# Performance work log

Hardware: AMD Instinct MI355X
Metric: run time of the kernel (lower is better)

## Reference

```python
import jax, jax.numpy as jnp
import numpy as np

B, NQ, NK = 16, 2048, 2048
KD, QD, KQ = 256, 256, 256
CLIP = 10.0


def setup_inputs() -> dict:
    key = jax.random.key(0)
    k1, k2, k3, k4, k5 = jax.random.split(key, 5)
    k_inputs = jax.random.normal(k1, (B, NK, KD), dtype=jnp.float32)
    q_inputs = jax.random.normal(k2, (B, NQ, QD), dtype=jnp.float32)
    adjancy = jax.random.randint(k3, (B, NQ, NK), 0, 2, dtype=jnp.int32)
    # Linear init in source: (rand - 0.5) * 0.05 -> uniform(-0.025, 0.025)
    Wk = jax.random.uniform(k4, (KD, KQ), dtype=jnp.float32, minval=-0.025, maxval=0.025)
    Wq = jax.random.uniform(k5, (QD, KQ), dtype=jnp.float32, minval=-0.025, maxval=0.025)
    return {"k_inputs": k_inputs, "q_inputs": q_inputs, "adjancy": adjancy, "Wk": Wk, "Wq": Wq}


def reference(k_inputs, q_inputs, adjancy, Wk, Wq):
    k = jnp.einsum("bnd,de->bne", k_inputs, Wk)          # [B, NK, KQ]
    q = jnp.einsum("bmd,de->bme", q_inputs, Wq)          # [B, NQ, KQ]
    scale = 1.0 / jnp.sqrt(jnp.asarray(KQ, dtype=q.dtype))
    scores = jnp.einsum("bme,bne->bmn", q, k) * scale     # [B, NQ, NK]
    scores = jnp.tanh(scores) * CLIP                      # clip is not None
    scores = jnp.where(adjancy.astype(bool), scores, -jnp.inf)
    return jax.nn.softmax(scores, axis=2)
```

## Files before the change

### kernel.cpp

```cpp
#include <hip/hip_runtime.h>

#define BATCH 16
#define NQ 2048
#define NK 2048
#define KD 256

typedef short s16x8 __attribute__((ext_vector_type(8)));
typedef __bf16 bf16x8 __attribute__((ext_vector_type(8)));
typedef float f32x16 __attribute__((ext_vector_type(16)));
typedef float f32x4 __attribute__((ext_vector_type(4)));

static __device__ __forceinline__ unsigned short f2bf(float f) {
  unsigned u = __builtin_bit_cast(unsigned, f);
  u += 0x7FFFu + ((u >> 16) & 1u);
  return (unsigned short)(u >> 16);
}

static __device__ __forceinline__ float bf2f(unsigned short h) {
  return __builtin_bit_cast(float, (unsigned)h << 16);
}

static __device__ __forceinline__ f32x16 mfma_bf16(s16x8 a, s16x8 b, f32x16 c) {
  return __builtin_amdgcn_mfma_f32_32x32x16_bf16(
      __builtin_bit_cast(bf16x8, a), __builtin_bit_cast(bf16x8, b), c, 0, 0, 0);
}

__global__ void prep_wt(const float* __restrict__ Wk, unsigned short* __restrict__ WkT,
                        const float* __restrict__ Wq, unsigned short* __restrict__ WqT) {
  const float* W = blockIdx.y ? Wq : Wk;
  unsigned short* WT = blockIdx.y ? WqT : WkT;
  float scale = blockIdx.y ? 0.0625f : 1.0f;
  int idx = blockIdx.x * 256 + threadIdx.x;
  int n = idx >> 8, k = idx & 255;
  WT[n * 256 + k] = f2bf(W[k * 256 + n] * scale);
}

__global__ __launch_bounds__(256, 2) void proj_kernel(
    const float* __restrict__ Xk, const unsigned short* __restrict__ WkT,
    unsigned short* __restrict__ Yk,
    const float* __restrict__ Xq, const unsigned short* __restrict__ WqT,
    unsigned short* __restrict__ Yq) {
  const float* X;
  const unsigned short* WT;
  unsigned short* Y;
  if (blockIdx.y == 0) { X = Xk; WT = WkT; Y = Yk; }
  else                 { X = Xq; WT = WqT; Y = Yq; }

  int tid = threadIdx.x;
  int wave = tid >> 6, lane = tid & 63;
  int l31 = lane & 31, kh = lane >> 5;
  int r0 = blockIdx.x * 128 + wave * 32;

  const float* xp = X + (size_t)(r0 + l31) * 256 + kh * 8;

  f32x16 acc[8];
#pragma unroll
  for (int ct = 0; ct < 8; ++ct)
#pragma unroll
    for (int i = 0; i < 16; ++i) acc[ct][i] = 0.0f;

#pragma unroll
  for (int kk = 0; kk < 16; ++kk) {
    f32x4 a0 = *(const f32x4*)(xp + kk * 16);
    f32x4 a1 = *(const f32x4*)(xp + kk * 16 + 4);
    s16x8 af;
#pragma unroll
    for (int j = 0; j < 4; ++j) {
      af[j]     = (short)f2bf(a0[j]);
      af[4 + j] = (short)f2bf(a1[j]);
    }
#pragma unroll
    for (int ct = 0; ct < 8; ++ct) {
      s16x8 bw = *(const s16x8*)(WT + (size_t)(ct * 32 + l31) * 256 + kk * 16 + kh * 8);
      acc[ct] = mfma_bf16(af, bw, acc[ct]);
    }
  }

  size_t gbase = (size_t)(r0 >> 5) * 16;
#pragma unroll
  for (int ct = 0; ct < 8; ++ct) {
    int ecol = ct * 32 + l31;
    size_t cbase = (gbase + (ecol >> 4)) * 64 * 8 + ((ecol >> 3) & 1) * 32 * 8 + (ecol & 7);
#pragma unroll
    for (int r = 0; r < 16; ++r) {
      int rrow = (r & 3) + 8 * (r >> 2) + 4 * kh;
      Y[cbase + rrow * 8] = f2bf(acc[ct][r]);
    }
  }
}

__global__ __launch_bounds__(512, 2) void attn_kernel(
    const unsigned short* __restrict__ Kf, const unsigned short* __restrict__ Qf,
    const int* __restrict__ adj, float* __restrict__ out) {
  int lin = blockIdx.y * 64 + blockIdx.x;
  int b  = (lin & 7) * 2 + ((lin >> 3) & 1);
  int qt = lin >> 4;
  int q0 = qt * 32;
  int tid = threadIdx.x;
  int wave = tid >> 6, lane = tid & 63;
  int l31 = lane & 31, kh = lane >> 5;
  int colbase = wave * 256;

  __shared__ unsigned lmask[8 * 256];
  __shared__ float wsum[8][32];
  __shared__ float rrecip[32];

  const unsigned short* qp = Qf + ((size_t)(b * 64 + qt) * 16) * 512;
  s16x8 aq[16];
#pragma unroll
  for (int kk = 0; kk < 16; ++kk)
    aq[kk] = *(const s16x8*)(qp + (kk * 64 + lane) * 8);

  const int* abase = adj + ((size_t)b * NQ + q0) * (size_t)NK + colbase + lane;
  unsigned* lm = lmask + wave * 256;
#pragma unroll
  for (int rg = 0; rg < 4; ++rg) {
    int av[8][4];
#pragma unroll
    for (int r8 = 0; r8 < 8; ++r8) {
      const int* ap = abase + (size_t)(rg * 8 + r8) * NK;
#pragma unroll
      for (int cc = 0; cc < 4; ++cc) av[r8][cc] = ap[cc * 64];
    }
#pragma unroll
    for (int r8 = 0; r8 < 8; ++r8) {
      unsigned long long b0 = __ballot(av[r8][0] != 0);
      unsigned long long b1 = __ballot(av[r8][1] != 0);
      unsigned long long b2 = __ballot(av[r8][2] != 0);
      unsigned long long b3 = __ballot(av[r8][3] != 0);
      if (lane < 8) {
        unsigned long long bb = (lane & 4) ? ((lane & 2) ? b3 : b2)
                                           : ((lane & 2) ? b1 : b0);
        unsigned word = (lane & 1) ? (unsigned)(bb >> 32) : (unsigned)bb;
        lm[(rg * 8 + r8) * 8 + lane] = word;
      }
    }
  }

  const unsigned short* kfb = Kf + ((size_t)b * 64 * 16) * 512;

  float rsum[16];
#pragma unroll
  for (int r = 0; r < 16; ++r) rsum[r] = 0.0f;

  s16x8 pst[8][2];
  unsigned bit = 1u << l31;

#pragma unroll
  for (int ct = 0; ct < 8; ++ct) {
    f32x16 acc;
#pragma unroll
    for (int i = 0; i < 16; ++i) acc[i] = 0.0f;

    const unsigned short* kpt = kfb + ((size_t)(wave * 8 + ct) * 16) * 512;
#pragma unroll
    for (int kk = 0; kk < 16; ++kk) {
      s16x8 bk = *(const s16x8*)(kpt + (kk * 64 + lane) * 8);
      acc = mfma_bf16(aq[kk], bk, acc);
    }

#pragma unroll
    for (int r = 0; r < 16; ++r) {
      int rrow = (r & 3) + 8 * (r >> 2) + 4 * kh;
      unsigned mw = lm[rrow * 8 + ct];
      float s = acc[r];
      float u  = __builtin_amdgcn_exp2f(s * 2.885390081777927f);
      float th = 1.0f - 2.0f * __builtin_amdgcn_rcpf(u + 1.0f);
      float e  = __builtin_amdgcn_exp2f((10.0f * th - 10.0f) * 1.44269504088896f);
      float p  = (mw & bit) ? e : 0.0f;
      rsum[r] += p;
      pst[ct][r >> 3][r & 7] = (short)f2bf(p);
    }
  }

#pragma unroll
  for (int r = 0; r < 16; ++r) {
    float v = rsum[r];
    v += __shfl_xor(v, 1);
    v += __shfl_xor(v, 2);
    v += __shfl_xor(v, 4);
    v += __shfl_xor(v, 8);
    v += __shfl_xor(v, 16);
    rsum[r] = v;
  }
  if (l31 == 0) {
#pragma unroll
    for (int r = 0; r < 16; ++r)
      wsum[wave][(r & 3) + 8 * (r >> 2) + 4 * kh] = rsum[r];
  }
  __syncthreads();
  if (tid < 32) {
    float s = 0.0f;
#pragma unroll
    for (int w = 0; w < 8; ++w) s += wsum[w][tid];
    rrecip[tid] = 1.0f / s;
  }
  __syncthreads();

  float rc[16];
#pragma unroll
  for (int r = 0; r < 16; ++r) rc[r] = rrecip[(r & 3) + 8 * (r >> 2) + 4 * kh];

  float* op = out + ((size_t)b * NQ + q0) * (size_t)NK + colbase + l31;
#pragma unroll
  for (int ct = 0; ct < 8; ++ct) {
#pragma unroll
    for (int r = 0; r < 16; ++r) {
      int rrow = (r & 3) + 8 * (r >> 2) + 4 * kh;
      float pf = bf2f((unsigned short)pst[ct][r >> 3][r & 7]);
      op[(size_t)rrow * NK + ct * 32] = pf * rc[r];
    }
  }
}

extern "C" void kernel_launch(void* const* d_in, const int* in_sizes, int n_in,
                              void* d_out, int out_size, void* d_ws, size_t ws_size,
                              hipStream_t stream) {
  const float* k_in = (const float*)d_in[0];
  const float* q_in = (const float*)d_in[1];
  const int* adj    = (const int*)d_in[2];
  const float* Wk   = (const float*)d_in[3];
  const float* Wq   = (const float*)d_in[4];
  float* out = (float*)d_out;

  char* ws = (char*)d_ws;
  unsigned short* WkT = (unsigned short*)(ws);
  unsigned short* WqT = (unsigned short*)(ws + (1u << 17));
  unsigned short* Kf  = (unsigned short*)(ws + (1u << 18));
  unsigned short* Qf  = (unsigned short*)(ws + (1u << 18) + (1u << 24));

  prep_wt<<<dim3(256, 2), 256, 0, stream>>>(Wk, WkT, Wq, WqT);

  proj_kernel<<<dim3(256, 2), 256, 0, stream>>>(k_in, WkT, Kf, q_in, WqT, Qf);

  attn_kernel<<<dim3(64, 16), 512, 0, stream>>>(Kf, Qf, adj, out);
}
```

Before: 260.5 us.

## Recompute attention scores in a second pass to cut registers and raise occupancy

The Q fragment moves from per-wave registers into shared memory, and the bf16 probability stash held between the row-sum pass and the output pass is dropped. The output pass now recomputes the QK^T MFMAs and the tanh/exp math instead of reading stored values. With far fewer live registers, launch bounds go from 2 to 4 blocks per CU to increase occupancy and hide memory latency. The cost is twice the MFMA and transcendental work plus repeated K loads from global memory and Q reads from LDS.

```diff
diff --git a/kernel.cpp b/kernel.cpp
--- a/kernel.cpp
+++ b/kernel.cpp
@@ -14,10 +14,6 @@
   unsigned u = __builtin_bit_cast(unsigned, f);
   u += 0x7FFFu + ((u >> 16) & 1u);
   return (unsigned short)(u >> 16);
-}
-
-static __device__ __forceinline__ float bf2f(unsigned short h) {
-  return __builtin_bit_cast(float, (unsigned)h << 16);
 }
 
 static __device__ __forceinline__ f32x16 mfma_bf16(s16x8 a, s16x8 b, f32x16 c) {
@@ -89,7 +85,7 @@
   }
 }
 
-__global__ __launch_bounds__(512, 2) void attn_kernel(
+__global__ __launch_bounds__(512, 4) void attn_kernel(
     const unsigned short* __restrict__ Kf, const unsigned short* __restrict__ Qf,
     const int* __restrict__ adj, float* __restrict__ out) {
   int lin = blockIdx.y * 64 + blockIdx.x;
@@ -101,15 +97,14 @@
   int l31 = lane & 31, kh = lane >> 5;
   int colbase = wave * 256;
 
+  __shared__ unsigned short qlds[16 * 512];
   __shared__ unsigned lmask[8 * 256];
   __shared__ float wsum[8][32];
   __shared__ float rrecip[32];
 
   const unsigned short* qp = Qf + ((size_t)(b * 64 + qt) * 16) * 512;
-  s16x8 aq[16];
-#pragma unroll
-  for (int kk = 0; kk < 16; ++kk)
-    aq[kk] = *(const s16x8*)(qp + (kk * 64 + lane) * 8);
+  ((s16x8*)qlds)[tid]       = ((const s16x8*)qp)[tid];
+  ((s16x8*)qlds)[tid + 512] = ((const s16x8*)qp)[tid + 512];
 
   const int* abase = adj + ((size_t)b * NQ + q0) * (size_t)NK + colbase + lane;
   unsigned* lm = lmask + wave * 256;
@@ -137,39 +132,36 @@
     }
   }
 
+  __syncthreads();
+
   const unsigned short* kfb = Kf + ((size_t)b * 64 * 16) * 512;
+  unsigned bit = 1u << l31;
 
   float rsum[16];
 #pragma unroll
   for (int r = 0; r < 16; ++r) rsum[r] = 0.0f;
-
-  s16x8 pst[8][2];
-  unsigned bit = 1u << l31;
 
 #pragma unroll
   for (int ct = 0; ct < 8; ++ct) {
     f32x16 acc;
 #pragma unroll
     for (int i = 0; i < 16; ++i) acc[i] = 0.0f;
-
     const unsigned short* kpt = kfb + ((size_t)(wave * 8 + ct) * 16) * 512;
 #pragma unroll
     for (int kk = 0; kk < 16; ++kk) {
+      s16x8 a  = *(const s16x8*)(qlds + (kk * 64 + lane) * 8);
       s16x8 bk = *(const s16x8*)(kpt + (kk * 64 + lane) * 8);
-      acc = mfma_bf16(aq[kk], bk, acc);
-    }
-
+      acc = mfma_bf16(a, bk, acc);
+    }
 #pragma unroll
     for (int r = 0; r < 16; ++r) {
       int rrow = (r & 3) + 8 * (r >> 2) + 4 * kh;
       unsigned mw = lm[rrow * 8 + ct];
-      float s = acc[r];
+      float s  = acc[r];
       float u  = __builtin_amdgcn_exp2f(s * 2.885390081777927f);
       float th = 1.0f - 2.0f * __builtin_amdgcn_rcpf(u + 1.0f);
       float e  = __builtin_amdgcn_exp2f((10.0f * th - 10.0f) * 1.44269504088896f);
-      float p  = (mw & bit) ? e : 0.0f;
-      rsum[r] += p;
-      pst[ct][r >> 3][r & 7] = (short)f2bf(p);
+      rsum[r] += (mw & bit) ? e : 0.0f;
     }
   }
 
@@ -204,11 +196,26 @@
   float* op = out + ((size_t)b * NQ + q0) * (size_t)NK + colbase + l31;
 #pragma unroll
   for (int ct = 0; ct < 8; ++ct) {
+    f32x16 acc;
+#pragma unroll
+    for (int i = 0; i < 16; ++i) acc[i] = 0.0f;
+    const unsigned short* kpt = kfb + ((size_t)(wave * 8 + ct) * 16) * 512;
+#pragma unroll
+    for (int kk = 0; kk < 16; ++kk) {
+      s16x8 a  = *(const s16x8*)(qlds + (kk * 64 + lane) * 8);
+      s16x8 bk = *(const s16x8*)(kpt + (kk * 64 + lane) * 8);
+      acc = mfma_bf16(a, bk, acc);
+    }
 #pragma unroll
     for (int r = 0; r < 16; ++r) {
       int rrow = (r & 3) + 8 * (r >> 2) + 4 * kh;
-      float pf = bf2f((unsigned short)pst[ct][r >> 3][r & 7]);
-      op[(size_t)rrow * NK + ct * 32] = pf * rc[r];
+      unsigned mw = lm[rrow * 8 + ct];
+      float s  = acc[r];
+      float u  = __builtin_amdgcn_exp2f(s * 2.885390081777927f);
+      float th = 1.0f - 2.0f * __builtin_amdgcn_rcpf(u + 1.0f);
+      float e  = __builtin_amdgcn_exp2f((10.0f * th - 10.0f) * 1.44269504088896f);
+      float p  = (mw & bit) ? e : 0.0f;
+      op[(size_t)rrow * NK + ct * 32] = p * rc[r];
     }
   }
 }
```

After: 905.9 us. 3.48x slower.

## Switch attention to 16x16 MFMA tiles with 16-row blocks and LDS-staged probabilities

Applied to the files above, without the earlier changes.

The attention kernel now handles 16 query rows per block instead of 32, using 16x16x32 bf16 MFMAs, and the launch grid doubles to match. The projection output layout is rearranged to fit the new fragment shape. Unnormalized probabilities are staged in LDS as packed bf16 instead of held in registers, and the tanh-plus-exp chain is folded into fewer operations. The aim is to cut register pressure and raise occupancy and parallelism, at the cost of re-reading each K tile twice as often overall and more LDS traffic.

```diff
diff --git a/kernel.cpp b/kernel.cpp
--- a/kernel.cpp
+++ b/kernel.cpp
@@ -3,12 +3,12 @@
 #define BATCH 16
 #define NQ 2048
 #define NK 2048
-#define KD 256
 
 typedef short s16x8 __attribute__((ext_vector_type(8)));
 typedef __bf16 bf16x8 __attribute__((ext_vector_type(8)));
 typedef float f32x16 __attribute__((ext_vector_type(16)));
 typedef float f32x4 __attribute__((ext_vector_type(4)));
+typedef unsigned u32x2 __attribute__((ext_vector_type(2)));
 
 static __device__ __forceinline__ unsigned short f2bf(float f) {
   unsigned u = __builtin_bit_cast(unsigned, f);
@@ -16,13 +16,19 @@
   return (unsigned short)(u >> 16);
 }
 
-static __device__ __forceinline__ float bf2f(unsigned short h) {
-  return __builtin_bit_cast(float, (unsigned)h << 16);
-}
-
-static __device__ __forceinline__ f32x16 mfma_bf16(s16x8 a, s16x8 b, f32x16 c) {
+static __device__ __forceinline__ f32x16 mfma32(s16x8 a, s16x8 b, f32x16 c) {
   return __builtin_amdgcn_mfma_f32_32x32x16_bf16(
       __builtin_bit_cast(bf16x8, a), __builtin_bit_cast(bf16x8, b), c, 0, 0, 0);
+}
+
+static __device__ __forceinline__ f32x4 mfma16(s16x8 a, s16x8 b, f32x4 c) {
+  return __builtin_amdgcn_mfma_f32_16x16x32_bf16(
+      __builtin_bit_cast(bf16x8, a), __builtin_bit_cast(bf16x8, b), c, 0, 0, 0);
+}
+
+static __device__ __forceinline__ float score_p(float s) {
+  float u = __builtin_amdgcn_exp2f(s * 2.885390081777927f);
+  return __builtin_amdgcn_exp2f(-28.853900817779268f * __builtin_amdgcn_rcpf(u + 1.0f));
 }
 
 __global__ void prep_wt(const float* __restrict__ Wk, unsigned short* __restrict__ WkT,
@@ -72,19 +78,19 @@
 #pragma unroll
     for (int ct = 0; ct < 8; ++ct) {
       s16x8 bw = *(const s16x8*)(WT + (size_t)(ct * 32 + l31) * 256 + kk * 16 + kh * 8);
-      acc[ct] = mfma_bf16(af, bw, acc[ct]);
-    }
-  }
-
-  size_t gbase = (size_t)(r0 >> 5) * 16;
+      acc[ct] = mfma32(af, bw, acc[ct]);
+    }
+  }
+
+  int kg2 = l31 >> 3, j = l31 & 7;
 #pragma unroll
   for (int ct = 0; ct < 8; ++ct) {
-    int ecol = ct * 32 + l31;
-    size_t cbase = (gbase + (ecol >> 4)) * 64 * 8 + ((ecol >> 3) & 1) * 32 * 8 + (ecol & 7);
 #pragma unroll
     for (int r = 0; r < 16; ++r) {
       int rrow = (r & 3) + 8 * (r >> 2) + 4 * kh;
-      Y[cbase + rrow * 8] = f2bf(acc[ct][r]);
+      int row = r0 + rrow;
+      Y[((size_t)((row >> 4) * 8 + ct) * 64 + kg2 * 16 + (row & 15)) * 8 + j] =
+          f2bf(acc[ct][r]);
     }
   }
 }
@@ -92,104 +98,88 @@
 __global__ __launch_bounds__(512, 2) void attn_kernel(
     const unsigned short* __restrict__ Kf, const unsigned short* __restrict__ Qf,
     const int* __restrict__ adj, float* __restrict__ out) {
-  int lin = blockIdx.y * 64 + blockIdx.x;
+  int lin = blockIdx.y * 128 + blockIdx.x;
   int b  = (lin & 7) * 2 + ((lin >> 3) & 1);
   int qt = lin >> 4;
-  int q0 = qt * 32;
+  int q0 = qt * 16;
   int tid = threadIdx.x;
   int wave = tid >> 6, lane = tid & 63;
-  int l31 = lane & 31, kh = lane >> 5;
+  int l15 = lane & 15, kg = lane >> 4;
   int colbase = wave * 256;
 
-  __shared__ unsigned lmask[8 * 256];
-  __shared__ float wsum[8][32];
-  __shared__ float rrecip[32];
-
-  const unsigned short* qp = Qf + ((size_t)(b * 64 + qt) * 16) * 512;
-  s16x8 aq[16];
-#pragma unroll
-  for (int kk = 0; kk < 16; ++kk)
-    aq[kk] = *(const s16x8*)(qp + (kk * 64 + lane) * 8);
+  __shared__ unsigned plds[8 * 16 * 64 * 2];
+  __shared__ unsigned lmask[8 * 144];
+  __shared__ float wsum[8][16];
+  __shared__ float rrecip[16];
+
+  const unsigned short* qp = Qf + (size_t)(b * 128 + qt) * 8 * 512;
+  s16x8 aq[8];
+#pragma unroll
+  for (int kk = 0; kk < 8; ++kk)
+    aq[kk] = *(const s16x8*)(qp + ((size_t)kk * 64 + lane) * 8);
 
   const int* abase = adj + ((size_t)b * NQ + q0) * (size_t)NK + colbase + lane;
-  unsigned* lm = lmask + wave * 256;
-#pragma unroll
-  for (int rg = 0; rg < 4; ++rg) {
-    int av[8][4];
-#pragma unroll
-    for (int r8 = 0; r8 < 8; ++r8) {
-      const int* ap = abase + (size_t)(rg * 8 + r8) * NK;
-#pragma unroll
-      for (int cc = 0; cc < 4; ++cc) av[r8][cc] = ap[cc * 64];
-    }
-#pragma unroll
-    for (int r8 = 0; r8 < 8; ++r8) {
-      unsigned long long b0 = __ballot(av[r8][0] != 0);
-      unsigned long long b1 = __ballot(av[r8][1] != 0);
-      unsigned long long b2 = __ballot(av[r8][2] != 0);
-      unsigned long long b3 = __ballot(av[r8][3] != 0);
-      if (lane < 8) {
-        unsigned long long bb = (lane & 4) ? ((lane & 2) ? b3 : b2)
-                                           : ((lane & 2) ? b1 : b0);
-        unsigned word = (lane & 1) ? (unsigned)(bb >> 32) : (unsigned)bb;
-        lm[(rg * 8 + r8) * 8 + lane] = word;
-      }
-    }
-  }
-
-  const unsigned short* kfb = Kf + ((size_t)b * 64 * 16) * 512;
-
-  float rsum[16];
-#pragma unroll
-  for (int r = 0; r < 16; ++r) rsum[r] = 0.0f;
-
-  s16x8 pst[8][2];
-  unsigned bit = 1u << l31;
-
-#pragma unroll
-  for (int ct = 0; ct < 8; ++ct) {
-    f32x16 acc;
-#pragma unroll
-    for (int i = 0; i < 16; ++i) acc[i] = 0.0f;
-
-    const unsigned short* kpt = kfb + ((size_t)(wave * 8 + ct) * 16) * 512;
-#pragma unroll
-    for (int kk = 0; kk < 16; ++kk) {
-      s16x8 bk = *(const s16x8*)(kpt + (kk * 64 + lane) * 8);
-      acc = mfma_bf16(aq[kk], bk, acc);
-    }
-
-#pragma unroll
-    for (int r = 0; r < 16; ++r) {
-      int rrow = (r & 3) + 8 * (r >> 2) + 4 * kh;
-      unsigned mw = lm[rrow * 8 + ct];
-      float s = acc[r];
-      float u  = __builtin_amdgcn_exp2f(s * 2.885390081777927f);
-      float th = 1.0f - 2.0f * __builtin_amdgcn_rcpf(u + 1.0f);
-      float e  = __builtin_amdgcn_exp2f((10.0f * th - 10.0f) * 1.44269504088896f);
-      float p  = (mw & bit) ? e : 0.0f;
-      rsum[r] += p;
-      pst[ct][r >> 3][r & 7] = (short)f2bf(p);
-    }
-  }
-
+  unsigned* lm = lmask + wave * 144;
 #pragma unroll
   for (int r = 0; r < 16; ++r) {
+    const int* ap = abase + (size_t)r * NK;
+    int a0 = ap[0], a1 = ap[64], a2 = ap[128], a3 = ap[192];
+    unsigned long long b0 = __ballot(a0 != 0);
+    unsigned long long b1 = __ballot(a1 != 0);
+    unsigned long long b2 = __ballot(a2 != 0);
+    unsigned long long b3 = __ballot(a3 != 0);
+    if (lane < 8) {
+      unsigned long long bb = (lane & 4) ? ((lane & 2) ? b3 : b2)
+                                         : ((lane & 2) ? b1 : b0);
+      unsigned word = (lane & 1) ? (unsigned)(bb >> 32) : (unsigned)bb;
+      lm[r * 9 + lane] = word;
+    }
+  }
+
+  const unsigned short* kfb = Kf + (size_t)b * 128 * 8 * 512;
+  unsigned* pl = plds + (wave * 16) * 128 + lane * 2;
+
+  float rsum[4] = {0.0f, 0.0f, 0.0f, 0.0f};
+
+#pragma unroll 2
+  for (int ct = 0; ct < 16; ++ct) {
+    f32x4 acc = {0.0f, 0.0f, 0.0f, 0.0f};
+    const unsigned short* kpt = kfb + (size_t)(wave * 16 + ct) * 8 * 512;
+#pragma unroll
+    for (int kk = 0; kk < 8; ++kk) {
+      s16x8 bk = *(const s16x8*)(kpt + ((size_t)kk * 64 + lane) * 8);
+      acc = mfma16(aq[kk], bk, acc);
+    }
+    unsigned shift = (unsigned)((ct & 1) * 16 + l15);
+    float p[4];
+#pragma unroll
+    for (int r = 0; r < 4; ++r) {
+      unsigned mw = lm[(kg * 4 + r) * 9 + (ct >> 1)];
+      float e = score_p(acc[r]);
+      p[r] = ((mw >> shift) & 1u) ? e : 0.0f;
+      rsum[r] += p[r];
+    }
+    unsigned lo = (unsigned)f2bf(p[0]) | ((unsigned)f2bf(p[1]) << 16);
+    unsigned hi = (unsigned)f2bf(p[2]) | ((unsigned)f2bf(p[3]) << 16);
+    u32x2 v; v[0] = lo; v[1] = hi;
+    *(u32x2*)(pl + ct * 128) = v;
+  }
+
+#pragma unroll
+  for (int r = 0; r < 4; ++r) {
     float v = rsum[r];
     v += __shfl_xor(v, 1);
     v += __shfl_xor(v, 2);
     v += __shfl_xor(v, 4);
     v += __shfl_xor(v, 8);
-    v += __shfl_xor(v, 16);
     rsum[r] = v;
   }
-  if (l31 == 0) {
-#pragma unroll
-    for (int r = 0; r < 16; ++r)
-      wsum[wave][(r & 3) + 8 * (r >> 2) + 4 * kh] = rsum[r];
+  if (l15 == 0) {
+#pragma unroll
+    for (int r = 0; r < 4; ++r) wsum[wave][kg * 4 + r] = rsum[r];
   }
   __syncthreads();
-  if (tid < 32) {
+  if (tid < 16) {
     float s = 0.0f;
 #pragma unroll
     for (int w = 0; w < 8; ++w) s += wsum[w][tid];
@@ -197,19 +187,22 @@
   }
   __syncthreads();
 
-  float rc[16];
-#pragma unroll
-  for (int r = 0; r < 16; ++r) rc[r] = rrecip[(r & 3) + 8 * (r >> 2) + 4 * kh];
-
-  float* op = out + ((size_t)b * NQ + q0) * (size_t)NK + colbase + l31;
-#pragma unroll
-  for (int ct = 0; ct < 8; ++ct) {
-#pragma unroll
-    for (int r = 0; r < 16; ++r) {
-      int rrow = (r & 3) + 8 * (r >> 2) + 4 * kh;
-      float pf = bf2f((unsigned short)pst[ct][r >> 3][r & 7]);
-      op[(size_t)rrow * NK + ct * 32] = pf * rc[r];
-    }
+  float rc[4];
+#pragma unroll
+  for (int r = 0; r < 4; ++r) rc[r] = rrecip[kg * 4 + r];
+
+  float* op = out + ((size_t)b * NQ + q0 + kg * 4) * (size_t)NK + colbase + l15;
+#pragma unroll 4
+  for (int ct = 0; ct < 16; ++ct) {
+    u32x2 v = *(const u32x2*)(pl + ct * 128);
+    float p0 = __builtin_bit_cast(float, v[0] << 16);
+    float p1 = __builtin_bit_cast(float, v[0] & 0xffff0000u);
+    float p2 = __builtin_bit_cast(float, v[1] << 16);
+    float p3 = __builtin_bit_cast(float, v[1] & 0xffff0000u);
+    op[(size_t)0 * NK + ct * 16] = p0 * rc[0];
+    op[(size_t)1 * NK + ct * 16] = p1 * rc[1];
+    op[(size_t)2 * NK + ct * 16] = p2 * rc[2];
+    op[(size_t)3 * NK + ct * 16] = p3 * rc[3];
   }
 }
 
@@ -233,5 +226,5 @@
 
   proj_kernel<<<dim3(256, 2), 256, 0, stream>>>(k_in, WkT, Kf, q_in, WqT, Qf);
 
-  attn_kernel<<<dim3(64, 16), 512, 0, stream>>>(Kf, Qf, adj, out);
-}
+  attn_kernel<<<dim3(128, 16), 512, 0, stream>>>(Kf, Qf, adj, out);
+}
```

Result: no change. 255.8 us (-1.8%).
